# Optimization experiments

Hardware: AMD Instinct MI355X
Metric: run time of the kernel (lower is better)

The kernel has to match this reference:

```python
import jax, jax.numpy as jnp
import numpy as np

N_S, N_H, N_ACT, N_LINKS = 512, 256, 7, 9
AXIS_LIST = jnp.array([2, 0, 2, 2, 2, 0, 2])
LINK_LIST = jnp.arange(N_ACT)
ROT_SIGN = jnp.array([1., 1., 1., 1., -1., 1., 1.], dtype=jnp.float32)  # rot[..., 4] *= -1
MASS = jnp.array([105.98, 105.98, 314.98, 279.2, 105.98, 105.98, 243.66], dtype=jnp.float32)
TOTAL_MASS = jnp.sum(MASS) + 100000.0 + 243.66
DIAGS = jnp.array([[12.19, 12.19, 3.061], [12.19, 12.19, 3.061], [15.41, 2094.71, 2103.19],
                   [9.522, 1966.28, 1966.28], [8.305, 3.061, 8.0386], [12.13, 12.13, 3.061],
                   [9.336, 44.41, 44.41]], dtype=jnp.float32)
INERTIAL = DIAGS[:, :, None] * jnp.eye(3, dtype=jnp.float32)          # (7,3,3) diagonal inertias
SUM_MASS = jnp.cumsum(MASS[::-1])[::-1].reshape(1, 1, 1, N_ACT)       # suffix sums
SUM_INERTIAL = jnp.cumsum(INERTIAL[::-1], axis=0)[::-1]               # (7,3,3)
TRIL = jnp.tril(jnp.ones((N_ACT, N_ACT), dtype=jnp.float32)).reshape(1, 1, N_ACT, 1, N_ACT)
MASS_MASK = MASS.reshape(1, 1, N_ACT, 1, 1) * TRIL                    # mass_H_wphi_mask
TF0 = jnp.array([[1, 0, 0, 0], [0, -1, 0, 0], [0, 0, 1.3, 6], [0, 0, 0, 1]], dtype=jnp.float32)
COM0 = jnp.array([[1, 0, 0, 0], [0, 1, 0, 0], [0, 0, 1, 0.5], [0, 0, 0, 1]], dtype=jnp.float32)
BASE_COM = (TF0 @ COM0)[:3, 3] * 243.66 / (100000.0 + 243.66)


def _skew(p):
    x, y, z = p[..., 0], p[..., 1], p[..., 2]
    z0 = jnp.zeros_like(x)
    return jnp.stack([jnp.stack([z0, -z, y], -1),
                      jnp.stack([z, z0, -x], -1),
                      jnp.stack([-y, x, z0], -1)], -2)


def _skew_mul(p):
    x, y, z = p[..., 0], p[..., 1], p[..., 2]
    r2 = x * x + y * y + z * z
    row0 = jnp.stack([r2 - x * x, -x * y, -x * z], -1)
    row1 = jnp.stack([-x * y, r2 - y * y, -y * z], -1)
    row2 = jnp.stack([-x * z, -y * z, r2 - z * z], -1)
    return jnp.stack([row0, row1, row2], -2)


def _inv3(H):
    a, b, c = H[..., 0, 0], H[..., 0, 1], H[..., 0, 2]
    d, e, f = H[..., 1, 0], H[..., 1, 1], H[..., 1, 2]
    g, h, i = H[..., 2, 0], H[..., 2, 1], H[..., 2, 2]
    det = a * (e * i - f * h) - b * (d * i - f * g) + c * (d * h - e * g)
    C11 = e * i - f * h; C12 = -(b * i - c * h); C13 = b * f - c * e
    C21 = -(d * i - f * g); C22 = a * i - c * g; C23 = -(a * f - c * d)
    C31 = d * h - e * g; C32 = -(a * h - b * g); C33 = a * e - b * d
    adj = jnp.stack([jnp.stack([C11, C21, C31], -1),
                     jnp.stack([C12, C22, C32], -1),
                     jnp.stack([C13, C23, C33], -1)], -2)
    return adj / det[..., None, None]


def _forward(com_list, link_pose_list, bm):
    rot = link_pose_list[:, :, :3, AXIS_LIST, LINK_LIST] * ROT_SIGN  # (n,h,3,7)
    if bm:
        del_p = com_list[:, :, :, :N_ACT] - link_pose_list[:, :, :3, 3, :N_ACT]  # (n,h,3,7)
        del_p_a = jnp.swapaxes(del_p, -1, -2)                                     # (n,h,7,3)
        del_p_skew = _skew(del_p_a)                                               # (n,h,7,3,3)
        jacob_t = jnp.cross(rot, del_p, axis=2)                                   # (n,h,3,7)
        jacob_tw = jacob_t * SUM_MASS
        H_w = jnp.sum(INERTIAL.reshape(1, 1, N_ACT, 3, 3)
                      + MASS.reshape(1, 1, N_ACT, 1, 1) * _skew_mul(del_p_a), axis=2)  # (n,h,3,3)
        term1 = jnp.einsum('aij,shja->shia', SUM_INERTIAL, rot)                   # (n,h,3,7)
        jac_w = jacob_t[:, :, None] * MASS_MASK                                   # (n,h,7,3,7)
        term2 = jnp.einsum('shaij,shajk->shik', del_p_skew, jac_w)                # (n,h,3,7)
        H_wphi = term1 + term2
        system_com = jnp.einsum('ntci,i->ntc', com_list, MASS) / TOTAL_MASS       # (n,h,3)
        r_og = _skew(system_com - BASE_COM)                                       # (n,h,3,3)
        H_s = TOTAL_MASS * (r_og @ r_og) + H_w
        H_theta = H_wphi - r_og @ jacob_tw
        H_inv = _inv3(H_s)
        top = -(jacob_tw / TOTAL_MASS + r_og @ (H_inv @ H_theta))
        bot = -(H_inv @ H_theta)
        return jnp.concatenate([top, bot], axis=2)                                # (n,h,6,7)
    else:
        del_p = link_pose_list[:, :, :3, 3, -2][..., None] - link_pose_list[:, :, :3, 3, :N_ACT]
        jt = jnp.cross(rot, del_p, axis=2)
        return jnp.concatenate([jt, rot], axis=2)


def setup_inputs() -> dict:
    key = jax.random.key(0)
    k1, k2 = jax.random.split(key)
    com_list = jax.random.normal(k1, (N_S, N_H, 3, N_ACT), dtype=jnp.float32)
    link_pose_list = jax.random.normal(k2, (N_S, N_H, 4, 4, N_LINKS), dtype=jnp.float32)
    return {"com_list": com_list, "link_pose_list": link_pose_list, "bm": 1}


def reference(com_list, link_pose_list, bm):
    return _forward(com_list, link_pose_list, bm)
```

## Files before the change

### kernel.cpp

```cpp
#include <hip/hip_runtime.h>


#define BLK 64

typedef const __attribute__((address_space(1))) void GAS;
typedef __attribute__((address_space(3))) void LAS;

__global__ __launch_bounds__(BLK, 1) void canadarm_jacob_kernel(
    const float* __restrict__ com,
    const float* __restrict__ pose,
    const int* __restrict__ bm_ptr,
    float* __restrict__ out)
{
    __shared__ float4 pose_lds[BLK * 21];
    __shared__ float4 com_lds[384];

    const int tid = threadIdx.x;
    const int item0 = blockIdx.x * BLK;

    const float MASS[7] = {105.98f, 105.98f, 314.98f, 279.2f, 105.98f, 105.98f, 243.66f};
    const float SUMM[7] = {1261.76f, 1155.78f, 1049.80f, 734.82f, 455.62f, 349.64f, 243.66f};
    const float SIX[7] = {79.083f, 66.893f, 54.703f, 39.293f, 29.771f, 21.466f, 9.336f};
    const float SIY[7] = {4144.971f, 4132.781f, 4120.591f, 2025.881f, 59.601f, 56.540f, 44.410f};
    const float SIZ[7] = {4131.1016f, 4128.0406f, 4124.9796f, 2021.7896f, 55.5096f, 47.471f, 44.410f};
    const float TM     = 101505.42f;
    const float INV_TM = 1.0f / 101505.42f;
    const float BCZ    = 6.65f * 243.66f / 100243.66f;

    {
        const float4* Pb4 = reinterpret_cast<const float4*>(pose) + (size_t)item0 * 36;
#pragma unroll
        for (int i = 0; i < 21; ++i) {
            const int d    = i * BLK + tid;
            const int item = d / 21;
            const int li   = d - item * 21;
            const int r    = li / 7;
            const int q    = li - r * 7;
            const int off  = 9 * r + (q < 2 ? q : q + 2);
            __builtin_amdgcn_global_load_lds(
                (GAS*)(Pb4 + item * 36 + off),
                (LAS*)(pose_lds + i * BLK), 16, 0, 0);
        }
        const float4* Cb4 = reinterpret_cast<const float4*>(com) + (size_t)item0 * 21 / 4 * 4 / 4;
        const float4* Cb4x = reinterpret_cast<const float4*>(com + (size_t)item0 * 21);
#pragma unroll
        for (int i = 0; i < 6; ++i) {
            const int d  = i * BLK + tid;
            const int dc = d < 336 ? d : 335;
            __builtin_amdgcn_global_load_lds(
                (GAS*)(Cb4x + dc),
                (LAS*)(com_lds + i * BLK), 16, 0, 0);
        }
        (void)Cb4;
    }
    asm volatile("s_waitcnt vmcnt(0)" ::: "memory");
    __syncthreads();

    const float4* L = &pose_lds[tid * 21];
    float rot[3][7];
    float tr[3][8];
#pragma unroll
    for (int r = 0; r < 3; ++r) {
        const float4 q0 = L[7 * r + 0];
        const float4 q1 = L[7 * r + 1];
        const float4 q4 = L[7 * r + 2];
        const float4 q5 = L[7 * r + 3];
        const float4 q6 = L[7 * r + 4];
        const float4 q7 = L[7 * r + 5];
        const float4 q8 = L[7 * r + 6];
        rot[r][0] = q4.z;
        rot[r][1] = q0.y;
        rot[r][2] = q5.x;
        rot[r][3] = q5.y;
        rot[r][4] = -q5.z;
        rot[r][5] = q1.y;
        rot[r][6] = q6.x;
        tr[r][0] = q6.w;
        tr[r][1] = q7.x; tr[r][2] = q7.y; tr[r][3] = q7.z; tr[r][4] = q7.w;
        tr[r][5] = q8.x; tr[r][6] = q8.y; tr[r][7] = q8.z;
    }

    const int bm = bm_ptr[0];
    float o[42];

    if (bm) {
        const float* Cf = reinterpret_cast<const float*>(com_lds) + tid * 21;
        float cm[3][7];
#pragma unroll
        for (int r = 0; r < 3; ++r)
#pragma unroll
            for (int i = 0; i < 7; ++i) cm[r][i] = Cf[r * 7 + i];

        float scx = 0.f, scy = 0.f, scz = 0.f;
#pragma unroll
        for (int i = 0; i < 7; ++i) {
            scx += cm[0][i] * MASS[i];
            scy += cm[1][i] * MASS[i];
            scz += cm[2][i] * MASS[i];
        }
        const float vx = scx * INV_TM;
        const float vy = scy * INV_TM;
        const float vz = scz * INV_TM - BCZ;

        float dp[3][7], jt[3][7];
        float hxx = SIX[0], hyy = SIY[0], hzz = SIZ[0];
        float hxy = 0.f, hxz = 0.f, hyz = 0.f;
#pragma unroll
        for (int i = 0; i < 7; ++i) {
            const float x = cm[0][i] - tr[0][i];
            const float y = cm[1][i] - tr[1][i];
            const float z = cm[2][i] - tr[2][i];
            dp[0][i] = x; dp[1][i] = y; dp[2][i] = z;
            jt[0][i] = rot[1][i] * z - rot[2][i] * y;
            jt[1][i] = rot[2][i] * x - rot[0][i] * z;
            jt[2][i] = rot[0][i] * y - rot[1][i] * x;
            const float m = MASS[i];
            hxx += m * (y * y + z * z);
            hyy += m * (x * x + z * z);
            hzz += m * (x * x + y * y);
            hxy -= m * x * y;
            hxz -= m * x * z;
            hyz -= m * y * z;
        }

        float wx[7], wy[7], wz[7];
        wx[6] = MASS[6] * dp[0][6];
        wy[6] = MASS[6] * dp[1][6];
        wz[6] = MASS[6] * dp[2][6];
#pragma unroll
        for (int k = 5; k >= 0; --k) {
            wx[k] = wx[k + 1] + MASS[k] * dp[0][k];
            wy[k] = wy[k + 1] + MASS[k] * dp[1][k];
            wz[k] = wz[k + 1] + MASS[k] * dp[2][k];
        }

        const float vv = vx * vx + vy * vy + vz * vz;
        const float a  = hxx + TM * (vx * vx - vv);
        const float b  = hxy + TM * (vx * vy);
        const float c  = hxz + TM * (vx * vz);
        const float e  = hyy + TM * (vy * vy - vv);
        const float f  = hyz + TM * (vy * vz);
        const float i9 = hzz + TM * (vz * vz - vv);

        const float c11 = e * i9 - f * f;
        const float c12 = c * f - b * i9;
        const float c13 = b * f - e * c;
        const float det = a * c11 + b * c12 + c * c13;
        const float rdet = 1.0f / det;
        const float i00 = c11 * rdet;
        const float i01 = c12 * rdet;
        const float i02 = c13 * rdet;
        const float i11 = (a * i9 - c * c) * rdet;
        const float i12 = (c * b - a * f) * rdet;
        const float i22 = (a * e - b * b) * rdet;

#pragma unroll
        for (int k = 0; k < 7; ++k) {
            const float ux = wx[k] - SUMM[k] * vx;
            const float uy = wy[k] - SUMM[k] * vy;
            const float uz = wz[k] - SUMM[k] * vz;
            const float jx = jt[0][k], jy = jt[1][k], jz = jt[2][k];
            const float htx = SIX[k] * rot[0][k] + uy * jz - uz * jy;
            const float hty = SIY[k] * rot[1][k] + uz * jx - ux * jz;
            const float htz = SIZ[k] * rot[2][k] + ux * jy - uy * jx;
            const float bx = i00 * htx + i01 * hty + i02 * htz;
            const float by = i01 * htx + i11 * hty + i12 * htz;
            const float bz = i02 * htx + i12 * hty + i22 * htz;
            const float s = SUMM[k] * INV_TM;
            o[0 * 7 + k] = -(s * jx + vy * bz - vz * by);
            o[1 * 7 + k] = -(s * jy + vz * bx - vx * bz);
            o[2 * 7 + k] = -(s * jz + vx * by - vy * bx);
            o[3 * 7 + k] = -bx;
            o[4 * 7 + k] = -by;
            o[5 * 7 + k] = -bz;
        }
    } else {
#pragma unroll
        for (int k = 0; k < 7; ++k) {
            const float dx = tr[0][7] - tr[0][k];
            const float dy = tr[1][7] - tr[1][k];
            const float dz = tr[2][7] - tr[2][k];
            o[0 * 7 + k] = rot[1][k] * dz - rot[2][k] * dy;
            o[1 * 7 + k] = rot[2][k] * dx - rot[0][k] * dz;
            o[2 * 7 + k] = rot[0][k] * dy - rot[1][k] * dx;
            o[3 * 7 + k] = rot[0][k];
            o[4 * 7 + k] = rot[1][k];
            o[5 * 7 + k] = rot[2][k];
        }
    }

    __syncthreads();
    float* ldsf = reinterpret_cast<float*>(pose_lds);
#pragma unroll
    for (int j = 0; j < 42; ++j) ldsf[tid * 42 + j] = o[j];
    __syncthreads();

    {
        float4* Ob4 = reinterpret_cast<float4*>(out) + (size_t)blockIdx.x * (BLK * 42 / 4);
        const float4* Lf4 = reinterpret_cast<const float4*>(ldsf);
#pragma unroll
        for (int i = 0; i < 10; ++i) Ob4[tid + i * BLK] = Lf4[tid + i * BLK];
        if (tid < 672 - 10 * BLK)
            Ob4[tid + 10 * BLK] = Lf4[tid + 10 * BLK];
    }
}

extern "C" void kernel_launch(void* const* d_in, const int* in_sizes, int n_in,
                              void* d_out, int out_size, void* d_ws, size_t ws_size,
                              hipStream_t stream) {
    const float* com  = (const float*)d_in[0];
    const float* pose = (const float*)d_in[1];
    const int*   bm   = (const int*)d_in[2];
    float* out = (float*)d_out;

    const int n_items = in_sizes[0] / 21;
    const int grid = n_items / BLK;
    canadarm_jacob_kernel<<<grid, BLK, 0, stream>>>(com, pose, bm, out);
}
```

Baseline: 124.4 us.

## Use 256-thread blocks for cooperative load/store while one wave computes

Blocks grow from 64 to 256 threads while each block still handles 64 items. All four waves share the global-to-LDS loads of pose and com data and the output stores, but only the first wave does the per-item Jacobian math. The output buffer moves into its own shared array, which removes one barrier, and the launch bound no longer forces one block per CU. The aim is to spread memory instruction issue across more waves and raise occupancy, at the cost of three idle waves during the compute phase.

```diff
diff --git a/kernel.cpp b/kernel.cpp
--- a/kernel.cpp
+++ b/kernel.cpp
@@ -1,207 +1,211 @@
 #include <hip/hip_runtime.h>
 
 
-#define BLK 64
+#define BLK 256
+#define ITEMS 64
 
 typedef const __attribute__((address_space(1))) void GAS;
 typedef __attribute__((address_space(3))) void LAS;
 
-__global__ __launch_bounds__(BLK, 1) void canadarm_jacob_kernel(
+__global__ __launch_bounds__(BLK) void canadarm_jacob_kernel(
     const float* __restrict__ com,
     const float* __restrict__ pose,
     const int* __restrict__ bm_ptr,
     float* __restrict__ out)
 {
-    __shared__ float4 pose_lds[BLK * 21];
-    __shared__ float4 com_lds[384];
+    __shared__ float4 pose_lds[ITEMS * 21];
+    __shared__ float4 com_lds[336];
+    __shared__ float  out_lds[ITEMS * 42];
 
     const int tid = threadIdx.x;
-    const int item0 = blockIdx.x * BLK;
-
-    const float MASS[7] = {105.98f, 105.98f, 314.98f, 279.2f, 105.98f, 105.98f, 243.66f};
-    const float SUMM[7] = {1261.76f, 1155.78f, 1049.80f, 734.82f, 455.62f, 349.64f, 243.66f};
-    const float SIX[7] = {79.083f, 66.893f, 54.703f, 39.293f, 29.771f, 21.466f, 9.336f};
-    const float SIY[7] = {4144.971f, 4132.781f, 4120.591f, 2025.881f, 59.601f, 56.540f, 44.410f};
-    const float SIZ[7] = {4131.1016f, 4128.0406f, 4124.9796f, 2021.7896f, 55.5096f, 47.471f, 44.410f};
-    const float TM     = 101505.42f;
-    const float INV_TM = 1.0f / 101505.42f;
-    const float BCZ    = 6.65f * 243.66f / 100243.66f;
+    const int item0 = blockIdx.x * ITEMS;
 
     {
         const float4* Pb4 = reinterpret_cast<const float4*>(pose) + (size_t)item0 * 36;
 #pragma unroll
-        for (int i = 0; i < 21; ++i) {
-            const int d    = i * BLK + tid;
-            const int item = d / 21;
-            const int li   = d - item * 21;
-            const int r    = li / 7;
-            const int q    = li - r * 7;
-            const int off  = 9 * r + (q < 2 ? q : q + 2);
-            __builtin_amdgcn_global_load_lds(
-                (GAS*)(Pb4 + item * 36 + off),
-                (LAS*)(pose_lds + i * BLK), 16, 0, 0);
-        }
-        const float4* Cb4 = reinterpret_cast<const float4*>(com) + (size_t)item0 * 21 / 4 * 4 / 4;
-        const float4* Cb4x = reinterpret_cast<const float4*>(com + (size_t)item0 * 21);
-#pragma unroll
         for (int i = 0; i < 6; ++i) {
-            const int d  = i * BLK + tid;
-            const int dc = d < 336 ? d : 335;
-            __builtin_amdgcn_global_load_lds(
-                (GAS*)(Cb4x + dc),
-                (LAS*)(com_lds + i * BLK), 16, 0, 0);
-        }
-        (void)Cb4;
+            const int d = i * BLK + tid;
+            if (d < ITEMS * 21) {
+                const int item = d / 21;
+                const int li   = d - item * 21;
+                const int r    = li / 7;
+                const int q    = li - r * 7;
+                const int off  = 9 * r + (q < 2 ? q : q + 2);
+                __builtin_amdgcn_global_load_lds(
+                    (GAS*)(Pb4 + item * 36 + off),
+                    (LAS*)(pose_lds + d), 16, 0, 0);
+            }
+        }
+        const float4* Cb4 = reinterpret_cast<const float4*>(com + (size_t)item0 * 21);
+#pragma unroll
+        for (int i = 0; i < 2; ++i) {
+            const int c = i * BLK + tid;
+            if (c < 336) {
+                __builtin_amdgcn_global_load_lds(
+                    (GAS*)(Cb4 + c),
+                    (LAS*)(com_lds + c), 16, 0, 0);
+            }
+        }
     }
     asm volatile("s_waitcnt vmcnt(0)" ::: "memory");
     __syncthreads();
 
-    const float4* L = &pose_lds[tid * 21];
-    float rot[3][7];
-    float tr[3][8];
-#pragma unroll
-    for (int r = 0; r < 3; ++r) {
-        const float4 q0 = L[7 * r + 0];
-        const float4 q1 = L[7 * r + 1];
-        const float4 q4 = L[7 * r + 2];
-        const float4 q5 = L[7 * r + 3];
-        const float4 q6 = L[7 * r + 4];
-        const float4 q7 = L[7 * r + 5];
-        const float4 q8 = L[7 * r + 6];
-        rot[r][0] = q4.z;
-        rot[r][1] = q0.y;
-        rot[r][2] = q5.x;
-        rot[r][3] = q5.y;
-        rot[r][4] = -q5.z;
-        rot[r][5] = q1.y;
-        rot[r][6] = q6.x;
-        tr[r][0] = q6.w;
-        tr[r][1] = q7.x; tr[r][2] = q7.y; tr[r][3] = q7.z; tr[r][4] = q7.w;
-        tr[r][5] = q8.x; tr[r][6] = q8.y; tr[r][7] = q8.z;
+    if (tid < ITEMS) {
+        const float MASS[7] = {105.98f, 105.98f, 314.98f, 279.2f, 105.98f, 105.98f, 243.66f};
+        const float SUMM[7] = {1261.76f, 1155.78f, 1049.80f, 734.82f, 455.62f, 349.64f, 243.66f};
+        const float SIX[7] = {79.083f, 66.893f, 54.703f, 39.293f, 29.771f, 21.466f, 9.336f};
+        const float SIY[7] = {4144.971f, 4132.781f, 4120.591f, 2025.881f, 59.601f, 56.540f, 44.410f};
+        const float SIZ[7] = {4131.1016f, 4128.0406f, 4124.9796f, 2021.7896f, 55.5096f, 47.471f, 44.410f};
+        const float TM     = 101505.42f;
+        const float INV_TM = 1.0f / 101505.42f;
+        const float BCZ    = 6.65f * 243.66f / 100243.66f;
+
+        const float4* L = &pose_lds[tid * 21];
+        float rot[3][7];
+        float tr[3][8];
+#pragma unroll
+        for (int r = 0; r < 3; ++r) {
+            const float4 q0 = L[7 * r + 0];
+            const float4 q1 = L[7 * r + 1];
+            const float4 q4 = L[7 * r + 2];
+            const float4 q5 = L[7 * r + 3];
+            const float4 q6 = L[7 * r + 4];
+            const float4 q7 = L[7 * r + 5];
+            const float4 q8 = L[7 * r + 6];
+            rot[r][0] = q4.z;
+            rot[r][1] = q0.y;
+            rot[r][2] = q5.x;
+            rot[r][3] = q5.y;
+            rot[r][4] = -q5.z;
+            rot[r][5] = q1.y;
+            rot[r][6] = q6.x;
+            tr[r][0] = q6.w;
+            tr[r][1] = q7.x; tr[r][2] = q7.y; tr[r][3] = q7.z; tr[r][4] = q7.w;
+            tr[r][5] = q8.x; tr[r][6] = q8.y; tr[r][7] = q8.z;
+        }
+
+        const int bm = bm_ptr[0];
+        float o[42];
+
+        if (bm) {
+            const float* Cf = reinterpret_cast<const float*>(com_lds) + tid * 21;
+            float cm[3][7];
+#pragma unroll
+            for (int r = 0; r < 3; ++r)
+#pragma unroll
+                for (int i = 0; i < 7; ++i) cm[r][i] = Cf[r * 7 + i];
+
+            float scx = 0.f, scy = 0.f, scz = 0.f;
+#pragma unroll
+            for (int i = 0; i < 7; ++i) {
+                scx += cm[0][i] * MASS[i];
+                scy += cm[1][i] * MASS[i];
+                scz += cm[2][i] * MASS[i];
+            }
+            const float vx = scx * INV_TM;
+            const float vy = scy * INV_TM;
+            const float vz = scz * INV_TM - BCZ;
+
+            float dp[3][7], jt[3][7];
+            float hxx = SIX[0], hyy = SIY[0], hzz = SIZ[0];
+            float hxy = 0.f, hxz = 0.f, hyz = 0.f;
+#pragma unroll
+            for (int i = 0; i < 7; ++i) {
+                const float x = cm[0][i] - tr[0][i];
+                const float y = cm[1][i] - tr[1][i];
+                const float z = cm[2][i] - tr[2][i];
+                dp[0][i] = x; dp[1][i] = y; dp[2][i] = z;
+                jt[0][i] = rot[1][i] * z - rot[2][i] * y;
+                jt[1][i] = rot[2][i] * x - rot[0][i] * z;
+                jt[2][i] = rot[0][i] * y - rot[1][i] * x;
+                const float m = MASS[i];
+                hxx += m * (y * y + z * z);
+                hyy += m * (x * x + z * z);
+                hzz += m * (x * x + y * y);
+                hxy -= m * x * y;
+                hxz -= m * x * z;
+                hyz -= m * y * z;
+            }
+
+            float wx[7], wy[7], wz[7];
+            wx[6] = MASS[6] * dp[0][6];
+            wy[6] = MASS[6] * dp[1][6];
+            wz[6] = MASS[6] * dp[2][6];
+#pragma unroll
+            for (int k = 5; k >= 0; --k) {
+                wx[k] = wx[k + 1] + MASS[k] * dp[0][k];
+                wy[k] = wy[k + 1] + MASS[k] * dp[1][k];
+                wz[k] = wz[k + 1] + MASS[k] * dp[2][k];
+            }
+
+            const float vv = vx * vx + vy * vy + vz * vz;
+            const float a  = hxx + TM * (vx * vx - vv);
+            const float b  = hxy + TM * (vx * vy);
+            const float c  = hxz + TM * (vx * vz);
+            const float e  = hyy + TM * (vy * vy - vv);
+            const float f  = hyz + TM * (vy * vz);
+            const float i9 = hzz + TM * (vz * vz - vv);
+
+            const float c11 = e * i9 - f * f;
+            const float c12 = c * f - b * i9;
+            const float c13 = b * f - e * c;
+            const float det = a * c11 + b * c12 + c * c13;
+            const float rdet = 1.0f / det;
+            const float i00 = c11 * rdet;
+            const float i01 = c12 * rdet;
+            const float i02 = c13 * rdet;
+            const float i11 = (a * i9 - c * c) * rdet;
+            const float i12 = (c * b - a * f) * rdet;
+            const float i22 = (a * e - b * b) * rdet;
+
+#pragma unroll
+            for (int k = 0; k < 7; ++k) {
+                const float ux = wx[k] - SUMM[k] * vx;
+                const float uy = wy[k] - SUMM[k] * vy;
+                const float uz = wz[k] - SUMM[k] * vz;
+                const float jx = jt[0][k], jy = jt[1][k], jz = jt[2][k];
+                const float htx = SIX[k] * rot[0][k] + uy * jz - uz * jy;
+                const float hty = SIY[k] * rot[1][k] + uz * jx - ux * jz;
+                const float htz = SIZ[k] * rot[2][k] + ux * jy - uy * jx;
+                const float bx = i00 * htx + i01 * hty + i02 * htz;
+                const float by = i01 * htx + i11 * hty + i12 * htz;
+                const float bz = i02 * htx + i12 * hty + i22 * htz;
+                const float s = SUMM[k] * INV_TM;
+                o[0 * 7 + k] = -(s * jx + vy * bz - vz * by);
+                o[1 * 7 + k] = -(s * jy + vz * bx - vx * bz);
+                o[2 * 7 + k] = -(s * jz + vx * by - vy * bx);
+                o[3 * 7 + k] = -bx;
+                o[4 * 7 + k] = -by;
+                o[5 * 7 + k] = -bz;
+            }
+        } else {
+#pragma unroll
+            for (int k = 0; k < 7; ++k) {
+                const float dx = tr[0][7] - tr[0][k];
+                const float dy = tr[1][7] - tr[1][k];
+                const float dz = tr[2][7] - tr[2][k];
+                o[0 * 7 + k] = rot[1][k] * dz - rot[2][k] * dy;
+                o[1 * 7 + k] = rot[2][k] * dx - rot[0][k] * dz;
+                o[2 * 7 + k] = rot[0][k] * dy - rot[1][k] * dx;
+                o[3 * 7 + k] = rot[0][k];
+                o[4 * 7 + k] = rot[1][k];
+                o[5 * 7 + k] = rot[2][k];
+            }
+        }
+
+#pragma unroll
+        for (int j = 0; j < 42; ++j) out_lds[tid * 42 + j] = o[j];
     }
-
-    const int bm = bm_ptr[0];
-    float o[42];
-
-    if (bm) {
-        const float* Cf = reinterpret_cast<const float*>(com_lds) + tid * 21;
-        float cm[3][7];
-#pragma unroll
-        for (int r = 0; r < 3; ++r)
-#pragma unroll
-            for (int i = 0; i < 7; ++i) cm[r][i] = Cf[r * 7 + i];
-
-        float scx = 0.f, scy = 0.f, scz = 0.f;
-#pragma unroll
-        for (int i = 0; i < 7; ++i) {
-            scx += cm[0][i] * MASS[i];
-            scy += cm[1][i] * MASS[i];
-            scz += cm[2][i] * MASS[i];
-        }
-        const float vx = scx * INV_TM;
-        const float vy = scy * INV_TM;
-        const float vz = scz * INV_TM - BCZ;
-
-        float dp[3][7], jt[3][7];
-        float hxx = SIX[0], hyy = SIY[0], hzz = SIZ[0];
-        float hxy = 0.f, hxz = 0.f, hyz = 0.f;
-#pragma unroll
-        for (int i = 0; i < 7; ++i) {
-            const float x = cm[0][i] - tr[0][i];
-            const float y = cm[1][i] - tr[1][i];
-            const float z = cm[2][i] - tr[2][i];
-            dp[0][i] = x; dp[1][i] = y; dp[2][i] = z;
-            jt[0][i] = rot[1][i] * z - rot[2][i] * y;
-            jt[1][i] = rot[2][i] * x - rot[0][i] * z;
-            jt[2][i] = rot[0][i] * y - rot[1][i] * x;
-            const float m = MASS[i];
-            hxx += m * (y * y + z * z);
-            hyy += m * (x * x + z * z);
-            hzz += m * (x * x + y * y);
-            hxy -= m * x * y;
-            hxz -= m * x * z;
-            hyz -= m * y * z;
-        }
-
-        float wx[7], wy[7], wz[7];
-        wx[6] = MASS[6] * dp[0][6];
-        wy[6] = MASS[6] * dp[1][6];
-        wz[6] = MASS[6] * dp[2][6];
-#pragma unroll
-        for (int k = 5; k >= 0; --k) {
-            wx[k] = wx[k + 1] + MASS[k] * dp[0][k];
-            wy[k] = wy[k + 1] + MASS[k] * dp[1][k];
-            wz[k] = wz[k + 1] + MASS[k] * dp[2][k];
-        }
-
-        const float vv = vx * vx + vy * vy + vz * vz;
-        const float a  = hxx + TM * (vx * vx - vv);
-        const float b  = hxy + TM * (vx * vy);
-        const float c  = hxz + TM * (vx * vz);
-        const float e  = hyy + TM * (vy * vy - vv);
-        const float f  = hyz + TM * (vy * vz);
-        const float i9 = hzz + TM * (vz * vz - vv);
-
-        const float c11 = e * i9 - f * f;
-        const float c12 = c * f - b * i9;
-        const float c13 = b * f - e * c;
-        const float det = a * c11 + b * c12 + c * c13;
-        const float rdet = 1.0f / det;
-        const float i00 = c11 * rdet;
-        const float i01 = c12 * rdet;
-        const float i02 = c13 * rdet;
-        const float i11 = (a * i9 - c * c) * rdet;
-        const float i12 = (c * b - a * f) * rdet;
-        const float i22 = (a * e - b * b) * rdet;
-
-#pragma unroll
-        for (int k = 0; k < 7; ++k) {
-            const float ux = wx[k] - SUMM[k] * vx;
-            const float uy = wy[k] - SUMM[k] * vy;
-            const float uz = wz[k] - SUMM[k] * vz;
-            const float jx = jt[0][k], jy = jt[1][k], jz = jt[2][k];
-            const float htx = SIX[k] * rot[0][k] + uy * jz - uz * jy;
-            const float hty = SIY[k] * rot[1][k] + uz * jx - ux * jz;
-            const float htz = SIZ[k] * rot[2][k] + ux * jy - uy * jx;
-            const float bx = i00 * htx + i01 * hty + i02 * htz;
-            const float by = i01 * htx + i11 * hty + i12 * htz;
-            const float bz = i02 * htx + i12 * hty + i22 * htz;
-            const float s = SUMM[k] * INV_TM;
-            o[0 * 7 + k] = -(s * jx + vy * bz - vz * by);
-            o[1 * 7 + k] = -(s * jy + vz * bx - vx * bz);
-            o[2 * 7 + k] = -(s * jz + vx * by - vy * bx);
-            o[3 * 7 + k] = -bx;
-            o[4 * 7 + k] = -by;
-            o[5 * 7 + k] = -bz;
-        }
-    } else {
-#pragma unroll
-        for (int k = 0; k < 7; ++k) {
-            const float dx = tr[0][7] - tr[0][k];
-            const float dy = tr[1][7] - tr[1][k];
-            const float dz = tr[2][7] - tr[2][k];
-            o[0 * 7 + k] = rot[1][k] * dz - rot[2][k] * dy;
-            o[1 * 7 + k] = rot[2][k] * dx - rot[0][k] * dz;
-            o[2 * 7 + k] = rot[0][k] * dy - rot[1][k] * dx;
-            o[3 * 7 + k] = rot[0][k];
-            o[4 * 7 + k] = rot[1][k];
-            o[5 * 7 + k] = rot[2][k];
-        }
-    }
-
     __syncthreads();
-    float* ldsf = reinterpret_cast<float*>(pose_lds);
-#pragma unroll
-    for (int j = 0; j < 42; ++j) ldsf[tid * 42 + j] = o[j];
-    __syncthreads();
 
     {
-        float4* Ob4 = reinterpret_cast<float4*>(out) + (size_t)blockIdx.x * (BLK * 42 / 4);
-        const float4* Lf4 = reinterpret_cast<const float4*>(ldsf);
-#pragma unroll
-        for (int i = 0; i < 10; ++i) Ob4[tid + i * BLK] = Lf4[tid + i * BLK];
-        if (tid < 672 - 10 * BLK)
-            Ob4[tid + 10 * BLK] = Lf4[tid + 10 * BLK];
+        float4* Ob4 = reinterpret_cast<float4*>(out) + (size_t)blockIdx.x * (ITEMS * 42 / 4);
+        const float4* Lf4 = reinterpret_cast<const float4*>(out_lds);
+#pragma unroll
+        for (int i = 0; i < 3; ++i) {
+            const int s = i * BLK + tid;
+            if (s < ITEMS * 42 / 4) Ob4[s] = Lf4[s];
+        }
     }
 }
 
@@ -214,6 +218,6 @@
     float* out = (float*)d_out;
 
     const int n_items = in_sizes[0] / 21;
-    const int grid = n_items / BLK;
+    const int grid = n_items / ITEMS;
     canadarm_jacob_kernel<<<grid, BLK, 0, stream>>>(com, pose, bm, out);
 }
```

Measured after the change: 123.8 us. No clear change (-0.4%).
